# Optimization experiments

Measured on AMD Instinct MI355X. Metric: run time of the kernel, lower is better.

Reference implementation:

```python
import jax, jax.numpy as jnp
import numpy as np

N_NODES = 50000
N_EDGES = 800000
IN_C, HID, OUT_C = 128, 128, 16
N_GRAPHS = 128


def setup_inputs() -> dict:
    key = jax.random.key(0)
    ks = jax.random.split(key, 8)
    x = jax.random.normal(ks[0], (N_NODES, IN_C), dtype=jnp.float32)
    edge_index = jax.random.randint(ks[1], (2, N_EDGES), 0, N_NODES, dtype=jnp.int64)
    batch = jnp.sort(jax.random.randint(ks[2], (N_NODES,), 0, N_GRAPHS, dtype=jnp.int64))
    s1 = 1.0 / np.sqrt(IN_C)
    s2 = 1.0 / np.sqrt(HID)
    W1 = jax.random.normal(ks[3], (IN_C, HID), dtype=jnp.float32) * s1
    b1 = jnp.zeros((HID,), dtype=jnp.float32)
    W2 = jax.random.normal(ks[4], (HID, HID), dtype=jnp.float32) * s2
    b2 = jnp.zeros((HID,), dtype=jnp.float32)
    Wfc = jax.random.normal(ks[5], (HID, OUT_C), dtype=jnp.float32) * s2
    bfc = jnp.zeros((OUT_C,), dtype=jnp.float32)
    return {"x": x, "edge_index": edge_index, "batch": batch,
            "W1": W1, "b1": b1, "W2": W2, "b2": b2, "Wfc": Wfc, "bfc": bfc}


def _gcn_conv(x, W, b, src, dst, deg_inv_sqrt, n_nodes):
    # linear transform first (PyG order), then normalized sparse aggregation
    h = x @ W  # [N, H]
    norm = deg_inv_sqrt[src] * deg_inv_sqrt[dst]  # [E+N] (self-loops appended)
    msgs = h[src] * norm[:, None]  # [E+N, H] dominant gather
    agg = jax.ops.segment_sum(msgs, dst, num_segments=n_nodes)
    return agg + b


def reference(x, edge_index, batch, W1, b1, W2, b2, Wfc, bfc):
    n = x.shape[0]
    loops = jnp.arange(n, dtype=edge_index.dtype)
    src = jnp.concatenate([edge_index[0], loops])
    dst = jnp.concatenate([edge_index[1], loops])
    # symmetric normalization with self-loops: deg computed on dst
    deg = jax.ops.segment_sum(jnp.ones_like(src, dtype=x.dtype), dst, num_segments=n)
    deg_inv_sqrt = jnp.where(deg > 0, jax.lax.rsqrt(jnp.maximum(deg, 1.0)), 0.0)

    h = jax.nn.relu(_gcn_conv(x, W1, b1, src, dst, deg_inv_sqrt, n))
    h = jax.nn.relu(_gcn_conv(h, W2, b2, src, dst, deg_inv_sqrt, n))

    # global mean pool over graph ids
    sums = jax.ops.segment_sum(h, batch, num_segments=N_GRAPHS)
    counts = jax.ops.segment_sum(jnp.ones((n,), dtype=h.dtype), batch, num_segments=N_GRAPHS)
    pooled = sums / jnp.maximum(counts, 1.0)[:, None]  # [G, H]

    logits = pooled @ Wfc + bfc  # [G, OUT_C]
    return jax.nn.log_softmax(logits, axis=1)
```

## Files before the change

### kernel.cpp

```cpp
#include <hip/hip_runtime.h>

#define N_NODES  50000
#define N_EDGES  800000
#define HID      128
#define OUT_C    16
#define N_GRAPHS 128
#define MAXDEG   64
#define NSLICE   6250
#define EPB      8192
#define FILLB    784
#define GEMMB    782
#define PAD      136

typedef __attribute__((ext_vector_type(8))) short bf16x8;
typedef __attribute__((ext_vector_type(4))) float f32x4;
typedef __attribute__((ext_vector_type(8))) unsigned short us8;
typedef __attribute__((ext_vector_type(4))) unsigned short us4;

__device__ __forceinline__ unsigned short f2bf(float f) {
  unsigned u = __float_as_uint(f);
  u += 0x7fffu + ((u >> 16) & 1u);
  return (unsigned short)(u >> 16);
}

__device__ __forceinline__ void gemm_compute_store(
    unsigned short* sA, const float* __restrict__ W,
    unsigned short* __restrict__ T, int base) {
  const int tid = threadIdx.x;
  const int lane = tid & 63;
  const int w = tid >> 6;
  const int l15 = lane & 15;
  const int quad = lane >> 4;
  __syncthreads();

  f32x4 acc[4][2];
#pragma unroll
  for (int nt = 0; nt < 4; ++nt)
#pragma unroll
    for (int c = 0; c < 2; ++c) acc[nt][c] = (f32x4)(0.f);

  const int ct0 = w * 2;
  const int ncol = ct0 * 16 + l15;
#pragma unroll
  for (int ks = 0; ks < 4; ++ks) {
    const int koff = ks * 32 + quad * 8;
    bf16x8 a[4], bfr[2];
#pragma unroll
    for (int c = 0; c < 2; ++c) {
      const float* wp = W + (size_t)koff * HID + ncol + c * 16;
#pragma unroll
      for (int j = 0; j < 8; ++j) bfr[c][j] = (short)f2bf(wp[(size_t)j * HID]);
    }
#pragma unroll
    for (int nt = 0; nt < 4; ++nt)
      a[nt] = *(const bf16x8*)(sA + (nt * 16 + l15) * PAD + koff);
#pragma unroll
    for (int nt = 0; nt < 4; ++nt)
#pragma unroll
      for (int c = 0; c < 2; ++c)
        acc[nt][c] = __builtin_amdgcn_mfma_f32_16x16x32_bf16(a[nt], bfr[c], acc[nt][c], 0, 0, 0);
  }
  __syncthreads();

#pragma unroll
  for (int nt = 0; nt < 4; ++nt)
#pragma unroll
    for (int c = 0; c < 2; ++c)
#pragma unroll
      for (int r = 0; r < 4; ++r)
        sA[(nt * 16 + quad * 4 + r) * PAD + (ct0 + c) * 16 + l15] = f2bf(acc[nt][c][r]);
  __syncthreads();
#pragma unroll
  for (int i = 0; i < 4; ++i) {
    int idx = tid + i * 256;
    int nrow = idx >> 4;
    int col = (idx & 15) * 8;
    int node = base + nrow;
    if (node < N_NODES)
      *(us8*)(T + (size_t)node * HID + col) = *(const us8*)(sA + nrow * PAD + col);
  }
}

__device__ __forceinline__ void stage_a_f32(unsigned short* sA,
                                            const float* __restrict__ H, int base) {
#pragma unroll
  for (int i = 0; i < 8; ++i) {
    int idx = threadIdx.x + i * 256;
    int nrow = idx >> 5;
    int c4 = (idx & 31) * 4;
    float4 v = make_float4(0.f, 0.f, 0.f, 0.f);
    int node = base + nrow;
    if (node < N_NODES) v = *(const float4*)(H + (size_t)node * HID + c4);
    us4 b;
    b.x = f2bf(v.x); b.y = f2bf(v.y); b.z = f2bf(v.z); b.w = f2bf(v.w);
    *(us4*)(sA + nrow * PAD + c4) = b;
  }
}

__global__ __launch_bounds__(256) void mega_kernel(
    const int* __restrict__ src, const int* __restrict__ dst,
    int* __restrict__ deg, unsigned short* __restrict__ ell,
    const int* __restrict__ batch, int* __restrict__ start,
    const float* __restrict__ x, const float* __restrict__ W1,
    unsigned short* __restrict__ T) {
  __shared__ unsigned short sA[64 * PAD];
  int b = blockIdx.x;
  if (b < FILLB) {
    const int slice = b & 7;
    const int e0 = (b >> 3) * EPB;
    const int e1 = min(e0 + EPB, N_EDGES);
    const unsigned lo = slice * NSLICE;
    for (int e = e0 + threadIdx.x; e < e1; e += 256) {
      int d = __builtin_nontemporal_load(dst + e);
      if ((unsigned)(d - lo) < (unsigned)NSLICE) {
        int p = atomicAdd(&deg[d], 1);
        if (p < MAXDEG) ell[(d << 6) + p] = (unsigned short)src[e];
      }
    }
  } else if (b == FILLB) {
    int t = threadIdx.x;
    if (t <= N_GRAPHS) {
      int lo = 0, hi = N_NODES;
      while (lo < hi) {
        int mid = (lo + hi) >> 1;
        if (batch[mid] < t) lo = mid + 1; else hi = mid;
      }
      start[t] = lo;
    }
  } else {
    const int base = (b - FILLB - 1) * 64;
    stage_a_f32(sA, x, base);
    gemm_compute_store(sA, W1, T, base);
  }
}

__global__ __launch_bounds__(256) void gemm_bf16_kernel(
    const unsigned short* __restrict__ Hb, const float* __restrict__ W,
    unsigned short* __restrict__ T) {
  __shared__ unsigned short sA[64 * PAD];
  const int base = blockIdx.x * 64;
#pragma unroll
  for (int i = 0; i < 4; ++i) {
    int idx = threadIdx.x + i * 256;
    int nrow = idx >> 4;
    int col = (idx & 15) * 8;
    us8 v = (us8)(0);
    int node = base + nrow;
    if (node < N_NODES) v = *(const us8*)(Hb + (size_t)node * HID + col);
    *(us8*)(sA + nrow * PAD + col) = v;
  }
  gemm_compute_store(sA, W, T, base);
}

__global__ __launch_bounds__(256) void aggregate_kernel(
    const unsigned int* __restrict__ Tb, const unsigned short* __restrict__ ell,
    const int* __restrict__ deg, const float* __restrict__ bias,
    unsigned int* __restrict__ Hb) {
  int node = (blockIdx.x * blockDim.x + threadIdx.x) >> 6;
  int lane = threadIdx.x & 63;
  if (node >= N_NODES) return;
  int dn = deg[node];
  float dd = rsqrtf((float)dn + 1.0f);
  float2 b = ((const float2*)bias)[lane];
  unsigned sv = Tb[(size_t)node * 64 + lane];
  float wself = dd * dd;
  float ax = __int_as_float(sv << 16) * wself;
  float ay = __int_as_float(sv & 0xffff0000u) * wself;
  int m = min(dn, MAXDEG);
  int s0 = node << 6;
  int sidx = 0; float wv = 0.f;
  if (lane < m) {
    sidx = (int)ell[s0 + lane];
    wv = rsqrtf((float)deg[sidx] + 1.0f) * dd;
  }
  int j = 0;
  for (; j + 8 <= m; j += 8) {
#pragma unroll
    for (int q = 0; q < 8; ++q) {
      int s = __builtin_amdgcn_readlane(sidx, j + q);
      float w = __int_as_float(__builtin_amdgcn_readlane(__float_as_int(wv), j + q));
      unsigned t = Tb[(size_t)s * 64 + lane];
      ax += w * __int_as_float(t << 16);
      ay += w * __int_as_float(t & 0xffff0000u);
    }
  }
  for (; j < m; ++j) {
    int s = __builtin_amdgcn_readlane(sidx, j);
    float w = __int_as_float(__builtin_amdgcn_readlane(__float_as_int(wv), j));
    unsigned t = Tb[(size_t)s * 64 + lane];
    ax += w * __int_as_float(t << 16);
    ay += w * __int_as_float(t & 0xffff0000u);
  }
  float ox = fmaxf(ax + b.x, 0.f);
  float oy = fmaxf(ay + b.y, 0.f);
  Hb[(size_t)node * 64 + lane] =
      (unsigned)f2bf(ox) | ((unsigned)f2bf(oy) << 16);
}

__global__ __launch_bounds__(256) void pool_head_kernel(
    const unsigned int* __restrict__ Hb, const int* __restrict__ start,
    const float* __restrict__ Wfc, const float* __restrict__ bfc,
    float* __restrict__ out) {
  __shared__ float2 red[4][64];
  __shared__ float spool[HID];
  int g = blockIdx.x;
  int n0 = start[g], n1 = start[g + 1];
  int lane = threadIdx.x & 63, w = threadIdx.x >> 6;
  float ax = 0.f, ay = 0.f;
  for (int n = n0 + w; n < n1; n += 4) {
    unsigned h = Hb[(size_t)n * 64 + lane];
    ax += __int_as_float(h << 16);
    ay += __int_as_float(h & 0xffff0000u);
  }
  red[w][lane] = make_float2(ax, ay);
  __syncthreads();
  if (threadIdx.x < 64) {
    float2 a = red[0][lane], b1 = red[1][lane], c = red[2][lane], d = red[3][lane];
    float inv = 1.0f / fmaxf((float)(n1 - n0), 1.0f);
    spool[lane * 2]     = (a.x + b1.x + c.x + d.x) * inv;
    spool[lane * 2 + 1] = (a.y + b1.y + c.y + d.y) * inv;
  }
  __syncthreads();
  if (threadIdx.x < 64) {
    int o = lane & 15;
    float part = 0.f;
    for (int k = (lane >> 4); k < HID; k += 4)
      part += spool[k] * Wfc[k * OUT_C + o];
    part += __shfl_xor(part, 16);
    part += __shfl_xor(part, 32);
    float logit = part + bfc[o];
    float m = logit;
#pragma unroll
    for (int d = 8; d >= 1; d >>= 1) m = fmaxf(m, __shfl_xor(m, d, 16));
    float e = __expf(logit - m);
    float s = e;
#pragma unroll
    for (int d = 8; d >= 1; d >>= 1) s += __shfl_xor(s, d, 16);
    float r = logit - m - __logf(s);
    if (lane < 16) out[g * OUT_C + o] = r;
  }
}

extern "C" void kernel_launch(void* const* d_in, const int* in_sizes, int n_in,
                              void* d_out, int out_size, void* d_ws, size_t ws_size,
                              hipStream_t stream) {
  const float* x    = (const float*)d_in[0];
  const int*   ei   = (const int*)d_in[1];
  const int*   batch= (const int*)d_in[2];
  const float* W1   = (const float*)d_in[3];
  const float* b1   = (const float*)d_in[4];
  const float* W2   = (const float*)d_in[5];
  const float* b2   = (const float*)d_in[6];
  const float* Wfc  = (const float*)d_in[7];
  const float* bfc  = (const float*)d_in[8];
  float* out = (float*)d_out;
  const int* src = ei;
  const int* dst = ei + N_EDGES;

  char* p = (char*)d_ws;
  auto alloc = [&](size_t bytes) { char* r = p; p += (bytes + 255) & ~255ull; return r; };
  int*   degI   = (int*)alloc((size_t)N_NODES * 4);
  int*   start  = (int*)alloc((N_GRAPHS + 1) * 4);
  unsigned short* ell = (unsigned short*)alloc((size_t)N_NODES * MAXDEG * 2);
  unsigned short* T   = (unsigned short*)alloc((size_t)N_NODES * HID * 2);
  unsigned short* Hb  = (unsigned short*)alloc((size_t)N_NODES * HID * 2);

  hipMemsetAsync(degI, 0, (size_t)N_NODES * 4, stream);

  int agg_blocks = (N_NODES * 64 + 255) / 256;

  mega_kernel<<<FILLB + 1 + GEMMB, 256, 0, stream>>>(src, dst, degI, ell,
                                                     batch, start, x, W1, T);
  aggregate_kernel<<<agg_blocks, 256, 0, stream>>>((const unsigned int*)T, ell, degI, b1,
                                                   (unsigned int*)Hb);
  gemm_bf16_kernel<<<GEMMB, 256, 0, stream>>>(Hb, W2, T);
  aggregate_kernel<<<agg_blocks, 256, 0, stream>>>((const unsigned int*)T, ell, degI, b2,
                                                   (unsigned int*)Hb);
  pool_head_kernel<<<N_GRAPHS, 256, 0, stream>>>((const unsigned int*)Hb, start,
                                                 Wfc, bfc, out);
}
```

Before: 255.5 us.

## Fuse layer-1 aggregation with layer-2 GEMM in one kernel

Merges the first aggregate kernel and the second bf16 GEMM into a single 1024-thread kernel. Each block aggregates 64 nodes into shared memory, then runs the MFMA GEMM against W2 and writes into a new T2 buffer. This removes one launch and the global write and re-read of the intermediate hidden activations. In exchange, the large 1024-thread blocks may lower occupancy and latency hiding during the gather-heavy aggregation. W2 is also converted to bf16 redundantly in every block.

Result: slower. 261.4 us (+2.3%).

```diff
diff --git a/kernel.cpp b/kernel.cpp
--- a/kernel.cpp
+++ b/kernel.cpp
@@ -134,34 +134,12 @@
   }
 }
 
-__global__ __launch_bounds__(256) void gemm_bf16_kernel(
-    const unsigned short* __restrict__ Hb, const float* __restrict__ W,
-    unsigned short* __restrict__ T) {
-  __shared__ unsigned short sA[64 * PAD];
-  const int base = blockIdx.x * 64;
-#pragma unroll
-  for (int i = 0; i < 4; ++i) {
-    int idx = threadIdx.x + i * 256;
-    int nrow = idx >> 4;
-    int col = (idx & 15) * 8;
-    us8 v = (us8)(0);
-    int node = base + nrow;
-    if (node < N_NODES) v = *(const us8*)(Hb + (size_t)node * HID + col);
-    *(us8*)(sA + nrow * PAD + col) = v;
-  }
-  gemm_compute_store(sA, W, T, base);
-}
-
-__global__ __launch_bounds__(256) void aggregate_kernel(
-    const unsigned int* __restrict__ Tb, const unsigned short* __restrict__ ell,
-    const int* __restrict__ deg, const float* __restrict__ bias,
-    unsigned int* __restrict__ Hb) {
-  int node = (blockIdx.x * blockDim.x + threadIdx.x) >> 6;
-  int lane = threadIdx.x & 63;
-  if (node >= N_NODES) return;
+__device__ __forceinline__ void agg_node(
+    int node, int lane, const unsigned int* __restrict__ Tb,
+    const unsigned short* __restrict__ ell, const int* __restrict__ deg,
+    float bx, float by, float& ox, float& oy) {
   int dn = deg[node];
   float dd = rsqrtf((float)dn + 1.0f);
-  float2 b = ((const float2*)bias)[lane];
   unsigned sv = Tb[(size_t)node * 64 + lane];
   float wself = dd * dd;
   float ax = __int_as_float(sv << 16) * wself;
@@ -191,8 +169,83 @@
     ax += w * __int_as_float(t << 16);
     ay += w * __int_as_float(t & 0xffff0000u);
   }
-  float ox = fmaxf(ax + b.x, 0.f);
-  float oy = fmaxf(ay + b.y, 0.f);
+  ox = fmaxf(ax + bx, 0.f);
+  oy = fmaxf(ay + by, 0.f);
+}
+
+__global__ __launch_bounds__(1024) void agg_gemm_kernel(
+    const unsigned int* __restrict__ Tb, const unsigned short* __restrict__ ell,
+    const int* __restrict__ deg, const float* __restrict__ bias,
+    const float* __restrict__ W, unsigned short* __restrict__ T2) {
+  __shared__ unsigned short sA[64 * PAD];
+  const int tid = threadIdx.x;
+  const int lane = tid & 63;
+  const int w = tid >> 6;
+  const int l15 = lane & 15;
+  const int quad = lane >> 4;
+  const int base = blockIdx.x * 64;
+
+  float2 b = ((const float2*)bias)[lane];
+#pragma unroll
+  for (int i = 0; i < 4; ++i) {
+    int nrow = w * 4 + i;
+    int node = base + nrow;
+    unsigned packed = 0;
+    if (node < N_NODES) {
+      float ox, oy;
+      agg_node(node, lane, Tb, ell, deg, b.x, b.y, ox, oy);
+      packed = (unsigned)f2bf(ox) | ((unsigned)f2bf(oy) << 16);
+    }
+    *(unsigned*)(sA + nrow * PAD + lane * 2) = packed;
+  }
+  __syncthreads();
+
+  const int nt = w >> 2;
+  const int ct0 = (w & 3) * 2;
+  const int ncol = ct0 * 16 + l15;
+  f32x4 acc[2];
+  acc[0] = (f32x4)(0.f); acc[1] = (f32x4)(0.f);
+#pragma unroll
+  for (int ks = 0; ks < 4; ++ks) {
+    const int koff = ks * 32 + quad * 8;
+    bf16x8 a, bfr[2];
+#pragma unroll
+    for (int c = 0; c < 2; ++c) {
+      const float* wp = W + (size_t)koff * HID + ncol + c * 16;
+#pragma unroll
+      for (int j = 0; j < 8; ++j) bfr[c][j] = (short)f2bf(wp[(size_t)j * HID]);
+    }
+    a = *(const bf16x8*)(sA + (nt * 16 + l15) * PAD + koff);
+#pragma unroll
+    for (int c = 0; c < 2; ++c)
+      acc[c] = __builtin_amdgcn_mfma_f32_16x16x32_bf16(a, bfr[c], acc[c], 0, 0, 0);
+  }
+  __syncthreads();
+#pragma unroll
+  for (int c = 0; c < 2; ++c)
+#pragma unroll
+    for (int r = 0; r < 4; ++r)
+      sA[(nt * 16 + quad * 4 + r) * PAD + (ct0 + c) * 16 + l15] = f2bf(acc[c][r]);
+  __syncthreads();
+  {
+    int nrow = tid >> 4;
+    int col = (tid & 15) * 8;
+    int node = base + nrow;
+    if (node < N_NODES)
+      *(us8*)(T2 + (size_t)node * HID + col) = *(const us8*)(sA + nrow * PAD + col);
+  }
+}
+
+__global__ __launch_bounds__(256) void aggregate_kernel(
+    const unsigned int* __restrict__ Tb, const unsigned short* __restrict__ ell,
+    const int* __restrict__ deg, const float* __restrict__ bias,
+    unsigned int* __restrict__ Hb) {
+  int node = (blockIdx.x * blockDim.x + threadIdx.x) >> 6;
+  int lane = threadIdx.x & 63;
+  if (node >= N_NODES) return;
+  float2 b = ((const float2*)bias)[lane];
+  float ox, oy;
+  agg_node(node, lane, Tb, ell, deg, b.x, b.y, ox, oy);
   Hb[(size_t)node * 64 + lane] =
       (unsigned)f2bf(ox) | ((unsigned)f2bf(oy) << 16);
 }
@@ -263,6 +316,7 @@
   int*   start  = (int*)alloc((N_GRAPHS + 1) * 4);
   unsigned short* ell = (unsigned short*)alloc((size_t)N_NODES * MAXDEG * 2);
   unsigned short* T   = (unsigned short*)alloc((size_t)N_NODES * HID * 2);
+  unsigned short* T2  = (unsigned short*)alloc((size_t)N_NODES * HID * 2);
   unsigned short* Hb  = (unsigned short*)alloc((size_t)N_NODES * HID * 2);
 
   hipMemsetAsync(degI, 0, (size_t)N_NODES * 4, stream);
@@ -271,10 +325,9 @@
 
   mega_kernel<<<FILLB + 1 + GEMMB, 256, 0, stream>>>(src, dst, degI, ell,
                                                      batch, start, x, W1, T);
-  aggregate_kernel<<<agg_blocks, 256, 0, stream>>>((const unsigned int*)T, ell, degI, b1,
-                                                   (unsigned int*)Hb);
-  gemm_bf16_kernel<<<GEMMB, 256, 0, stream>>>(Hb, W2, T);
-  aggregate_kernel<<<agg_blocks, 256, 0, stream>>>((const unsigned int*)T, ell, degI, b2,
+  agg_gemm_kernel<<<GEMMB, 1024, 0, stream>>>((const unsigned int*)T, ell, degI,
+                                              b1, W2, T2);
+  aggregate_kernel<<<agg_blocks, 256, 0, stream>>>((const unsigned int*)T2, ell, degI, b2,
                                                    (unsigned int*)Hb);
   pool_head_kernel<<<N_GRAPHS, 256, 0, stream>>>((const unsigned int*)Hb, start,
                                                  Wfc, bfc, out);
```
